# Kernel tuning notes

Measured on AMD Instinct MI355X. Metric: run time of the kernel, lower is better.

Reference implementation:

```python
import jax, jax.numpy as jnp
import numpy as np

NINP = 1024
NHID = 1024
BATCH = 16384
EPS = 1e-5


def _ln(x, g, b):
    mu = jnp.mean(x, axis=-1, keepdims=True)
    var = jnp.mean(jnp.square(x - mu), axis=-1, keepdims=True)
    return (x - mu) * jax.lax.rsqrt(var + EPS) * g + b


def setup_inputs() -> dict:
    key = jax.random.key(0)
    ks = jax.random.split(key, 12)
    s_i = 1.0 / np.sqrt(NINP)
    s_h = 1.0 / np.sqrt(NHID)
    return {
        "inp": jax.random.normal(ks[0], (BATCH, NINP), jnp.float32),
        "hidden": jax.random.normal(ks[1], (BATCH, NHID), jnp.float32),
        "W_i2gate": jax.random.uniform(ks[2], (3 * NHID, NINP), jnp.float32, -s_i, s_i),
        "b_i2gate": jnp.zeros((3 * NHID,), jnp.float32),
        "W_h2gate": jax.random.uniform(ks[3], (3 * NHID, NHID), jnp.float32, -s_h, s_h),
        "b_h2gate": jnp.zeros((3 * NHID,), jnp.float32),
        "W_i2i": jax.random.uniform(ks[4], (NHID, NINP), jnp.float32, -s_i, s_i),
        "b_i2i": jnp.zeros((NHID,), jnp.float32),
        "W_i2h": jax.random.uniform(ks[5], (NHID, NINP), jnp.float32, -s_i, s_i),
        "b_i2h": jnp.zeros((NHID,), jnp.float32),
        "W_h2h": jax.random.uniform(ks[6], (NHID, NHID), jnp.float32, -s_h, s_h),
        "b_h2h": jnp.zeros((NHID,), jnp.float32),
        "g_ig": jnp.ones((3 * NHID,), jnp.float32),
        "be_ig": jnp.zeros((3 * NHID,), jnp.float32),
        "g_hg": jnp.ones((3 * NHID,), jnp.float32),
        "be_hg": jnp.zeros((3 * NHID,), jnp.float32),
        "g_ii": jnp.ones((NHID,), jnp.float32),
        "be_ii": jnp.zeros((NHID,), jnp.float32),
        "g_ih": jnp.ones((NHID,), jnp.float32),
        "be_ih": jnp.zeros((NHID,), jnp.float32),
        "g_hh": jnp.ones((NHID,), jnp.float32),
        "be_hh": jnp.zeros((NHID,), jnp.float32),
    }


def reference(inp, hidden, W_i2gate, b_i2gate, W_h2gate, b_h2gate,
              W_i2i, b_i2i, W_i2h, b_i2h, W_h2h, b_h2h,
              g_ig, be_ig, g_hg, be_hg, g_ii, be_ii,
              g_ih, be_ih, g_hh, be_hh):
    gate = jax.nn.sigmoid(
        _ln(inp @ W_i2gate.T + b_i2gate, g_ig, be_ig)
        + _ln(hidden @ W_h2gate.T + b_h2gate, g_hg, be_hg))
    r, z, g = jnp.split(gate, 3, axis=-1)
    Hx = _ln(inp @ W_i2i.T + b_i2i, g_ii, be_ii)
    xh = _ln(inp @ W_i2h.T + b_i2h, g_ih, be_ih)
    hh = _ln(hidden @ W_h2h.T + b_h2h, g_hh, be_hh)
    hidden_m = jnp.tanh((1.0 - r) * xh + r * hh)
    return ((1.0 - z) * hidden + z * hidden_m) * (1.0 - g) + g * Hx
```

## Files before the change

kernel.cpp:

```cpp
#include <hip/hip_runtime.h>

typedef __bf16 bf16_t;
typedef bf16_t bf16x8 __attribute__((ext_vector_type(8)));
typedef bf16_t bf16x4 __attribute__((ext_vector_type(4)));
typedef float f32x4 __attribute__((ext_vector_type(4)));

#define BATCH 16384
#define KDIM  1024
#define NCOLS 9216

#define BMg 256
#define BNg 256
#define BKg 64
#define NTg (KDIM / BKg)
#define NBN (NCOLS / BNg)

__global__ __launch_bounds__(256)
void cast_all(const float* __restrict__ Wig, const float* __restrict__ Wii,
              const float* __restrict__ Wih, const float* __restrict__ Whg,
              const float* __restrict__ Whh,
              const float* __restrict__ big, const float* __restrict__ bii,
              const float* __restrict__ bih, const float* __restrict__ bhg,
              const float* __restrict__ bhh,
              const float* __restrict__ inp, const float* __restrict__ hid,
              bf16_t* __restrict__ Wcat, float* __restrict__ bcat,
              bf16_t* __restrict__ inpb, bf16_t* __restrict__ hidb,
              int nact_units, int ntot)
{
  int u = blockIdx.x * 256 + threadIdx.x;
  if (u >= ntot) return;

  if (u < 2359296) {
    const float* src; int off;
    if      (u < 786432)  { src = Wig; off = u; }
    else if (u < 1048576) { src = Wii; off = u - 786432; }
    else if (u < 1310720) { src = Wih; off = u - 1048576; }
    else if (u < 2097152) { src = Whg; off = u - 1310720; }
    else                  { src = Whh; off = u - 2097152; }
    float4 v = reinterpret_cast<const float4*>(src)[off];
    bf16x4 o;
    o[0] = (bf16_t)v.x; o[1] = (bf16_t)v.y; o[2] = (bf16_t)v.z; o[3] = (bf16_t)v.w;
    reinterpret_cast<bf16x4*>(Wcat)[u] = o;
  } else if (u < 2361600) {
    int bu = u - 2359296;
    int i = bu * 4;
    const float* src; int off;
    if      (i < 3072) { src = big; off = i; }
    else if (i < 4096) { src = bii; off = i - 3072; }
    else if (i < 5120) { src = bih; off = i - 4096; }
    else if (i < 8192) { src = bhg; off = i - 5120; }
    else               { src = bhh; off = i - 8192; }
    reinterpret_cast<float4*>(bcat)[bu] = *reinterpret_cast<const float4*>(src + off);
  } else {
    int au = u - 2361600;
    const float* src; bf16_t* dst; int off;
    if (au < nact_units) { src = inp; dst = inpb; off = au; }
    else                 { src = hid; dst = hidb; off = au - nact_units; }
    float4 v = reinterpret_cast<const float4*>(src)[off];
    bf16x4 o;
    o[0] = (bf16_t)v.x; o[1] = (bf16_t)v.y; o[2] = (bf16_t)v.z; o[3] = (bf16_t)v.w;
    reinterpret_cast<bf16x4*>(dst)[off] = o;
  }
}

__global__ __launch_bounds__(256)
void cast_acts(const float* __restrict__ inp, const float* __restrict__ hid,
               bf16_t* __restrict__ inpb, bf16_t* __restrict__ hidb, int n4) {
  int i = blockIdx.x * 256 + threadIdx.x;
  if (i >= 2 * n4) return;
  const float* src = (i < n4) ? inp : hid;
  bf16_t* dst = (i < n4) ? inpb : hidb;
  int off = (i < n4) ? i : i - n4;
  float4 v = reinterpret_cast<const float4*>(src)[off];
  bf16x4 o;
  o[0] = (bf16_t)v.x; o[1] = (bf16_t)v.y; o[2] = (bf16_t)v.z; o[3] = (bf16_t)v.w;
  reinterpret_cast<bf16x4*>(dst)[off] = o;
}

__global__ __launch_bounds__(512, 1)
void gemm_preln(const bf16_t* __restrict__ inpb, const bf16_t* __restrict__ hidb,
                const bf16_t* __restrict__ Wcat, const float* __restrict__ bcat,
                bf16_t* __restrict__ preLN, int nbm)
{
  __shared__ alignas(16) char lds_raw[131072];

  const int tid  = threadIdx.x;
  const int wid  = tid >> 6;
  const int lane = tid & 63;
  const int fr   = lane & 15;
  const int kg   = lane >> 4;
  const int wr   = wid >> 2;
  const int wc   = wid & 3;

  const int nwg = nbm * NBN;
  int orig = blockIdx.x;
  int q_ = nwg >> 3, r_ = nwg & 7, xcd = orig & 7, idx = orig >> 3;
  int wg = (xcd < r_ ? xcd * (q_ + 1) : r_ * (q_ + 1) + (xcd - r_) * q_) + idx;
  const int bm = wg / NBN, bn = wg % NBN;
  const int row0 = bm * BMg, col0 = bn * BNg;
  const bf16_t* __restrict__ act = (col0 < 5120) ? inpb : hidb;
  const bf16_t* __restrict__ wgt = Wcat + (size_t)col0 * KDIM;

  const int r_st  = tid >> 2;
  const int k8_st = (tid & 3) ^ ((r_st >> 1) & 3);
  const bf16_t* pA = act + (size_t)(row0 + r_st) * KDIM + k8_st * 8;
  const bf16_t* pB = wgt + (size_t)r_st * KDIM + k8_st * 8;

  auto stage_half = [&](int mat, int h, int T) {
    const bf16_t* s = (mat ? pB : pA) + ((size_t)h * 128) * KDIM + T * BKg;
    char* d = lds_raw + ((T & 1) << 16) + (mat << 15) + (h << 14) + (wid << 10);
    __builtin_amdgcn_global_load_lds(
        (const __attribute__((address_space(1))) unsigned int*)s,
        (__attribute__((address_space(3))) unsigned int*)d, 16, 0, 0);
    __builtin_amdgcn_global_load_lds(
        (const __attribute__((address_space(1))) unsigned int*)(s + 32),
        (__attribute__((address_space(3))) unsigned int*)(d + 8192), 16, 0, 0);
  };

  int offA[4][2], offB[2][2];
  #pragma unroll
  for (int m = 0; m < 4; ++m)
    #pragma unroll
    for (int ks = 0; ks < 2; ++ks) {
      const int rowA = wr * 64 + m * 16 + fr;
      offA[m][ks] = ks * 8192 + rowA * 64 + ((kg ^ ((rowA >> 1) & 3)) << 4);
    }
  #pragma unroll
  for (int n = 0; n < 2; ++n)
    #pragma unroll
    for (int ks = 0; ks < 2; ++ks) {
      const int rowB = wc * 32 + n * 16 + fr;
      offB[n][ks] = ks * 8192 + rowB * 64 + ((kg ^ ((rowB >> 1) & 3)) << 4);
    }

  f32x4 acc[2][4][2][2] = {};

  stage_half(0, 0, 0); stage_half(1, 0, 0);
  stage_half(0, 1, 0); stage_half(1, 1, 0);
  stage_half(0, 0, 1); stage_half(1, 0, 1);
  asm volatile("s_waitcnt vmcnt(4)" ::: "memory");
  __builtin_amdgcn_s_barrier();

  for (int T = 0; T < NTg; ++T) {
    const int bufo = (T & 1) << 16;
    #pragma unroll
    for (int ph = 0; ph < 4; ++ph) {
      const int qm = ph >> 1, qn = ph & 1;
      bf16x8 a[4][2], b[2][2];
      #pragma unroll
      for (int m = 0; m < 4; ++m)
        #pragma unroll
        for (int ks = 0; ks < 2; ++ks)
          a[m][ks] = *(const bf16x8*)(lds_raw + bufo + qm * 16384 + offA[m][ks]);
      #pragma unroll
      for (int n = 0; n < 2; ++n)
        #pragma unroll
        for (int ks = 0; ks < 2; ++ks)
          b[n][ks] = *(const bf16x8*)(lds_raw + bufo + 32768 + qn * 16384 + offB[n][ks]);

      if      (ph == 0) { if (T + 1 < NTg) stage_half(0, 1, T + 1); }
      else if (ph == 1) { if (T + 1 < NTg) stage_half(1, 1, T + 1); }
      else if (ph == 2) { if (T + 2 < NTg) stage_half(0, 0, T + 2); }
      else              { if (T + 2 < NTg) stage_half(1, 0, T + 2); }

      __builtin_amdgcn_s_barrier();
      asm volatile("s_waitcnt lgkmcnt(0)" ::: "memory");
      __builtin_amdgcn_sched_barrier(0);

      __builtin_amdgcn_s_setprio(1);
      #pragma unroll
      for (int m = 0; m < 4; ++m)
        #pragma unroll
        for (int n = 0; n < 2; ++n)
          #pragma unroll
          for (int ks = 0; ks < 2; ++ks)
            acc[qm][m][qn][n] = __builtin_amdgcn_mfma_f32_16x16x32_bf16(
                a[m][ks], b[n][ks], acc[qm][m][qn][n], 0, 0, 0);
      __builtin_amdgcn_s_setprio(0);

      if (ph < 3) __builtin_amdgcn_s_barrier();
    }
    if (T < NTg - 2) {
      asm volatile("s_waitcnt vmcnt(4)" ::: "memory");
      __builtin_amdgcn_s_barrier();
    } else if (T == NTg - 2) {
      asm volatile("s_waitcnt vmcnt(0)" ::: "memory");
      __builtin_amdgcn_s_barrier();
    }
  }

  #pragma unroll
  for (int qn_ = 0; qn_ < 2; ++qn_)
    #pragma unroll
    for (int n = 0; n < 2; ++n) {
      const int col = col0 + qn_ * 128 + wc * 32 + n * 16 + fr;
      const float bias = bcat[col];
      #pragma unroll
      for (int qm_ = 0; qm_ < 2; ++qm_)
        #pragma unroll
        for (int m = 0; m < 4; ++m) {
          const int rbase = row0 + qm_ * 128 + wr * 64 + m * 16 + kg * 4;
          #pragma unroll
          for (int j = 0; j < 4; ++j)
            preLN[(size_t)(rbase + j) * NCOLS + col] = (bf16_t)(acc[qm_][m][qn_][n][j] + bias);
        }
    }
}

__global__ __launch_bounds__(256)
void ln_combine(const bf16_t* __restrict__ preLN, const float* __restrict__ hidden,
                const float* __restrict__ g_ig, const float* __restrict__ be_ig,
                const float* __restrict__ g_hg, const float* __restrict__ be_hg,
                const float* __restrict__ g_ii, const float* __restrict__ be_ii,
                const float* __restrict__ g_ih, const float* __restrict__ be_ih,
                const float* __restrict__ g_hh, const float* __restrict__ be_hh,
                float* __restrict__ out)
{
  __shared__ alignas(16) bf16_t rowbuf[NCOLS];
  __shared__ float wsum[4][10];
  __shared__ float stats[10];
  const int tid = threadIdx.x;
  const int wv  = tid >> 6;
  const int ln  = tid & 63;
  const size_t row = blockIdx.x;
  const bf16_t* __restrict__ src = preLN + row * NCOLS;

  float s1[5] = {0.f, 0.f, 0.f, 0.f, 0.f};
  float s2[5] = {0.f, 0.f, 0.f, 0.f, 0.f};
  #pragma unroll
  for (int j = 0; j < 9; ++j) {
    const int idx = j * 1024 + tid * 4;
    bf16x4 v = *(const bf16x4*)&src[idx];
    *(bf16x4*)&rowbuf[idx] = v;
    const int sg = (j < 3) ? 0 : (j == 3) ? 1 : (j == 4) ? 2 : (j < 8) ? 3 : 4;
    const float f0 = (float)v[0], f1 = (float)v[1], f2 = (float)v[2], f3 = (float)v[3];
    s1[sg] += f0 + f1 + f2 + f3;
    s2[sg] += f0 * f0 + f1 * f1 + f2 * f2 + f3 * f3;
  }
  #pragma unroll
  for (int s = 0; s < 5; ++s)
    #pragma unroll
    for (int off = 32; off; off >>= 1) {
      s1[s] += __shfl_xor(s1[s], off);
      s2[s] += __shfl_xor(s2[s], off);
    }
  if (ln == 0) {
    #pragma unroll
    for (int s = 0; s < 5; ++s) { wsum[wv][s] = s1[s]; wsum[wv][5 + s] = s2[s]; }
  }
  __syncthreads();
  if (tid < 5) {
    const float n = (tid == 0 || tid == 3) ? 3072.f : 1024.f;
    float t1 = wsum[0][tid] + wsum[1][tid] + wsum[2][tid] + wsum[3][tid];
    float t2 = wsum[0][5 + tid] + wsum[1][5 + tid] + wsum[2][5 + tid] + wsum[3][5 + tid];
    float mu = t1 / n;
    float var = t2 / n - mu * mu;
    stats[tid] = mu;
    stats[5 + tid] = rsqrtf(var + 1e-5f);
  }
  __syncthreads();

  const float mu0 = stats[0], r0 = stats[5];
  const float mu1 = stats[1], r1 = stats[6];
  const float mu2 = stats[2], r2 = stats[7];
  const float mu3 = stats[3], r3 = stats[8];
  const float mu4 = stats[4], r4 = stats[9];
  const float* __restrict__ hrow = hidden + row * 1024;

  #pragma unroll
  for (int k = 0; k < 4; ++k) {
    const int c = tid + k * 256;
    float x_igr = (float)rowbuf[c];
    float x_igz = (float)rowbuf[c + 1024];
    float x_igg = (float)rowbuf[c + 2048];
    float x_ii  = (float)rowbuf[3072 + c];
    float x_ih  = (float)rowbuf[4096 + c];
    float x_hgr = (float)rowbuf[5120 + c];
    float x_hgz = (float)rowbuf[6144 + c];
    float x_hgg = (float)rowbuf[7168 + c];
    float x_hh  = (float)rowbuf[8192 + c];

    float pr = (x_igr - mu0) * r0 * g_ig[c]        + be_ig[c]
             + (x_hgr - mu3) * r3 * g_hg[c]        + be_hg[c];
    float pz = (x_igz - mu0) * r0 * g_ig[c + 1024] + be_ig[c + 1024]
             + (x_hgz - mu3) * r3 * g_hg[c + 1024] + be_hg[c + 1024];
    float pg = (x_igg - mu0) * r0 * g_ig[c + 2048] + be_ig[c + 2048]
             + (x_hgg - mu3) * r3 * g_hg[c + 2048] + be_hg[c + 2048];

    float rr = 1.f / (1.f + __expf(-pr));
    float zz = 1.f / (1.f + __expf(-pz));
    float gg = 1.f / (1.f + __expf(-pg));

    float Hx = (x_ii - mu1) * r1 * g_ii[c] + be_ii[c];
    float xh = (x_ih - mu2) * r2 * g_ih[c] + be_ih[c];
    float hh = (x_hh - mu4) * r4 * g_hh[c] + be_hh[c];

    float hm = tanhf((1.f - rr) * xh + rr * hh);
    float h  = hrow[c];
    out[row * 1024 + c] = ((1.f - zz) * h + zz * hm) * (1.f - gg) + gg * Hx;
  }
}

extern "C" void kernel_launch(void* const* d_in, const int* in_sizes, int n_in,
                              void* d_out, int out_size, void* d_ws, size_t ws_size,
                              hipStream_t stream) {
  const float* inp      = (const float*)d_in[0];
  const float* hidden   = (const float*)d_in[1];
  const float* W_i2gate = (const float*)d_in[2];
  const float* b_i2gate = (const float*)d_in[3];
  const float* W_h2gate = (const float*)d_in[4];
  const float* b_h2gate = (const float*)d_in[5];
  const float* W_i2i    = (const float*)d_in[6];
  const float* b_i2i    = (const float*)d_in[7];
  const float* W_i2h    = (const float*)d_in[8];
  const float* b_i2h    = (const float*)d_in[9];
  const float* W_h2h    = (const float*)d_in[10];
  const float* b_h2h    = (const float*)d_in[11];
  const float* g_ig  = (const float*)d_in[12];
  const float* be_ig = (const float*)d_in[13];
  const float* g_hg  = (const float*)d_in[14];
  const float* be_hg = (const float*)d_in[15];
  const float* g_ii  = (const float*)d_in[16];
  const float* be_ii = (const float*)d_in[17];
  const float* g_ih  = (const float*)d_in[18];
  const float* be_ih = (const float*)d_in[19];
  const float* g_hh  = (const float*)d_in[20];
  const float* be_hh = (const float*)d_in[21];
  float* out = (float*)d_out;

  const size_t WCAT_B  = (size_t)NCOLS * KDIM * 2;
  const size_t BCAT_B  = (size_t)NCOLS * 4;
  const size_t FIXED_B = WCAT_B + BCAT_B;
  const size_t PER_ROW = 2048 + 2048 + 18432;

  if (ws_size < FIXED_B + PER_ROW * 256) return;

  char* ws = (char*)d_ws;
  bf16_t* Wcat = (bf16_t*)ws;
  float*  bcat = (float*)(ws + WCAT_B);
  char*   dyn  = ws + FIXED_B;

  size_t max_rows = (ws_size - FIXED_B) / PER_ROW;
  int chunk = (int)((max_rows / 256) * 256);
  if (chunk > BATCH) chunk = BATCH;

  bf16_t* inpb  = (bf16_t*)dyn;
  bf16_t* hidb  = (bf16_t*)(dyn + (size_t)chunk * 2048);
  bf16_t* preLN = (bf16_t*)(dyn + (size_t)chunk * 4096);

  if (chunk == BATCH) {
    const int nact = BATCH * KDIM / 4;
    const int ntot = 2361600 + 2 * nact;
    cast_all<<<(ntot + 255) / 256, 256, 0, stream>>>(
        W_i2gate, W_i2i, W_i2h, W_h2gate, W_h2h,
        b_i2gate, b_i2i, b_i2h, b_h2gate, b_h2h,
        inp, hidden, Wcat, bcat, inpb, hidb, nact, ntot);

    int nbm = BATCH / BMg;
    gemm_preln<<<nbm * NBN, 512, 0, stream>>>(inpb, hidb, Wcat, bcat, preLN, nbm);

    ln_combine<<<BATCH, 256, 0, stream>>>(preLN, hidden,
                                          g_ig, be_ig, g_hg, be_hg,
                                          g_ii, be_ii, g_ih, be_ih, g_hh, be_hh,
                                          out);
  } else {
    const int ntot_w = 2361600;
    cast_all<<<(ntot_w + 255) / 256, 256, 0, stream>>>(
        W_i2gate, W_i2i, W_i2h, W_h2gate, W_h2h,
        b_i2gate, b_i2i, b_i2h, b_h2gate, b_h2h,
        nullptr, nullptr, Wcat, bcat, nullptr, nullptr, 0, ntot_w);

    for (int r0 = 0; r0 < BATCH; r0 += chunk) {
      int cr = BATCH - r0;
      if (cr > chunk) cr = chunk;
      int n4 = cr * KDIM / 4;
      cast_acts<<<(2 * n4 + 255) / 256, 256, 0, stream>>>(
          inp + (size_t)r0 * KDIM, hidden + (size_t)r0 * KDIM, inpb, hidb, n4);

      int nbm = cr / BMg;
      gemm_preln<<<nbm * NBN, 512, 0, stream>>>(inpb, hidb, Wcat, bcat, preLN, nbm);

      ln_combine<<<cr, 256, 0, stream>>>(preLN, hidden + (size_t)r0 * KDIM,
                                         g_ig, be_ig, g_hg, be_hg,
                                         g_ii, be_ii, g_ih, be_ih, g_hh, be_hh,
                                         out + (size_t)r0 * KDIM);
    }
  }
}
```

Baseline: 535.2 us.

## Reorder GEMM phases to reuse A/B fragments, raise occupancy hint, vectorize LN epilogue

The GEMM inner loop is reordered into a snake pattern (qm0qn0, qm0qn1, qm1qn1, qm1qn0), so A and B register fragments are reused across phases and fewer LDS reads are issued. The last phase also drops its lgkmcnt wait. The launch bounds are changed to request 2 waves per SIMD, which caps registers, though 128KB of LDS per block likely still limits the kernel to one block per CU. Separately, the LayerNorm/GRU epilogue is vectorized with 4-wide loads and stores, and tanhf is replaced by an exp-based formula. The register cap risks spills, and the fast tanh loses a little accuracy.

```diff
diff --git a/kernel.cpp b/kernel.cpp
--- a/kernel.cpp
+++ b/kernel.cpp
@@ -77,7 +77,7 @@
   reinterpret_cast<bf16x4*>(dst)[off] = o;
 }
 
-__global__ __launch_bounds__(512, 1)
+__global__ __launch_bounds__(512, 2)
 void gemm_preln(const bf16_t* __restrict__ inpb, const bf16_t* __restrict__ hidb,
                 const bf16_t* __restrict__ Wcat, const float* __restrict__ bcat,
                 bf16_t* __restrict__ preLN, int nbm)
@@ -143,43 +143,85 @@
 
   for (int T = 0; T < NTg; ++T) {
     const int bufo = (T & 1) << 16;
-    #pragma unroll
-    for (int ph = 0; ph < 4; ++ph) {
-      const int qm = ph >> 1, qn = ph & 1;
-      bf16x8 a[4][2], b[2][2];
-      #pragma unroll
-      for (int m = 0; m < 4; ++m)
-        #pragma unroll
-        for (int ks = 0; ks < 2; ++ks)
-          a[m][ks] = *(const bf16x8*)(lds_raw + bufo + qm * 16384 + offA[m][ks]);
+    bf16x8 a[4][2], b0[2][2], b1[2][2];
+
+    #pragma unroll
+    for (int m = 0; m < 4; ++m)
+      #pragma unroll
+      for (int ks = 0; ks < 2; ++ks)
+        a[m][ks] = *(const bf16x8*)(lds_raw + bufo + offA[m][ks]);
+    #pragma unroll
+    for (int n = 0; n < 2; ++n)
+      #pragma unroll
+      for (int ks = 0; ks < 2; ++ks)
+        b0[n][ks] = *(const bf16x8*)(lds_raw + bufo + 32768 + offB[n][ks]);
+    if (T + 1 < NTg) stage_half(0, 1, T + 1);
+    __builtin_amdgcn_s_barrier();
+    asm volatile("s_waitcnt lgkmcnt(0)" ::: "memory");
+    __builtin_amdgcn_sched_barrier(0);
+    __builtin_amdgcn_s_setprio(1);
+    #pragma unroll
+    for (int m = 0; m < 4; ++m)
       #pragma unroll
       for (int n = 0; n < 2; ++n)
         #pragma unroll
         for (int ks = 0; ks < 2; ++ks)
-          b[n][ks] = *(const bf16x8*)(lds_raw + bufo + 32768 + qn * 16384 + offB[n][ks]);
-
-      if      (ph == 0) { if (T + 1 < NTg) stage_half(0, 1, T + 1); }
-      else if (ph == 1) { if (T + 1 < NTg) stage_half(1, 1, T + 1); }
-      else if (ph == 2) { if (T + 2 < NTg) stage_half(0, 0, T + 2); }
-      else              { if (T + 2 < NTg) stage_half(1, 0, T + 2); }
-
-      __builtin_amdgcn_s_barrier();
-      asm volatile("s_waitcnt lgkmcnt(0)" ::: "memory");
-      __builtin_amdgcn_sched_barrier(0);
-
-      __builtin_amdgcn_s_setprio(1);
-      #pragma unroll
-      for (int m = 0; m < 4; ++m)
+          acc[0][m][0][n] = __builtin_amdgcn_mfma_f32_16x16x32_bf16(a[m][ks], b0[n][ks], acc[0][m][0][n], 0, 0, 0);
+    __builtin_amdgcn_s_setprio(0);
+    __builtin_amdgcn_s_barrier();
+
+    #pragma unroll
+    for (int n = 0; n < 2; ++n)
+      #pragma unroll
+      for (int ks = 0; ks < 2; ++ks)
+        b1[n][ks] = *(const bf16x8*)(lds_raw + bufo + 32768 + 16384 + offB[n][ks]);
+    if (T + 1 < NTg) stage_half(1, 1, T + 1);
+    __builtin_amdgcn_s_barrier();
+    asm volatile("s_waitcnt lgkmcnt(0)" ::: "memory");
+    __builtin_amdgcn_sched_barrier(0);
+    __builtin_amdgcn_s_setprio(1);
+    #pragma unroll
+    for (int m = 0; m < 4; ++m)
+      #pragma unroll
+      for (int n = 0; n < 2; ++n)
         #pragma unroll
-        for (int n = 0; n < 2; ++n)
-          #pragma unroll
-          for (int ks = 0; ks < 2; ++ks)
-            acc[qm][m][qn][n] = __builtin_amdgcn_mfma_f32_16x16x32_bf16(
-                a[m][ks], b[n][ks], acc[qm][m][qn][n], 0, 0, 0);
-      __builtin_amdgcn_s_setprio(0);
-
-      if (ph < 3) __builtin_amdgcn_s_barrier();
-    }
+        for (int ks = 0; ks < 2; ++ks)
+          acc[0][m][1][n] = __builtin_amdgcn_mfma_f32_16x16x32_bf16(a[m][ks], b1[n][ks], acc[0][m][1][n], 0, 0, 0);
+    __builtin_amdgcn_s_setprio(0);
+    __builtin_amdgcn_s_barrier();
+
+    #pragma unroll
+    for (int m = 0; m < 4; ++m)
+      #pragma unroll
+      for (int ks = 0; ks < 2; ++ks)
+        a[m][ks] = *(const bf16x8*)(lds_raw + bufo + 16384 + offA[m][ks]);
+    if (T + 2 < NTg) stage_half(0, 0, T + 2);
+    __builtin_amdgcn_s_barrier();
+    asm volatile("s_waitcnt lgkmcnt(0)" ::: "memory");
+    __builtin_amdgcn_sched_barrier(0);
+    __builtin_amdgcn_s_setprio(1);
+    #pragma unroll
+    for (int m = 0; m < 4; ++m)
+      #pragma unroll
+      for (int n = 0; n < 2; ++n)
+        #pragma unroll
+        for (int ks = 0; ks < 2; ++ks)
+          acc[1][m][1][n] = __builtin_amdgcn_mfma_f32_16x16x32_bf16(a[m][ks], b1[n][ks], acc[1][m][1][n], 0, 0, 0);
+    __builtin_amdgcn_s_setprio(0);
+    __builtin_amdgcn_s_barrier();
+
+    if (T + 2 < NTg) stage_half(1, 0, T + 2);
+    __builtin_amdgcn_s_barrier();
+    __builtin_amdgcn_s_setprio(1);
+    #pragma unroll
+    for (int m = 0; m < 4; ++m)
+      #pragma unroll
+      for (int n = 0; n < 2; ++n)
+        #pragma unroll
+        for (int ks = 0; ks < 2; ++ks)
+          acc[1][m][0][n] = __builtin_amdgcn_mfma_f32_16x16x32_bf16(a[m][ks], b0[n][ks], acc[1][m][0][n], 0, 0, 0);
+    __builtin_amdgcn_s_setprio(0);
+
     if (T < NTg - 2) {
       asm volatile("s_waitcnt vmcnt(4)" ::: "memory");
       __builtin_amdgcn_s_barrier();
@@ -267,38 +309,51 @@
   const float mu4 = stats[4], r4 = stats[9];
   const float* __restrict__ hrow = hidden + row * 1024;
 
-  #pragma unroll
-  for (int k = 0; k < 4; ++k) {
-    const int c = tid + k * 256;
-    float x_igr = (float)rowbuf[c];
-    float x_igz = (float)rowbuf[c + 1024];
-    float x_igg = (float)rowbuf[c + 2048];
-    float x_ii  = (float)rowbuf[3072 + c];
-    float x_ih  = (float)rowbuf[4096 + c];
-    float x_hgr = (float)rowbuf[5120 + c];
-    float x_hgz = (float)rowbuf[6144 + c];
-    float x_hgg = (float)rowbuf[7168 + c];
-    float x_hh  = (float)rowbuf[8192 + c];
-
-    float pr = (x_igr - mu0) * r0 * g_ig[c]        + be_ig[c]
-             + (x_hgr - mu3) * r3 * g_hg[c]        + be_hg[c];
-    float pz = (x_igz - mu0) * r0 * g_ig[c + 1024] + be_ig[c + 1024]
-             + (x_hgz - mu3) * r3 * g_hg[c + 1024] + be_hg[c + 1024];
-    float pg = (x_igg - mu0) * r0 * g_ig[c + 2048] + be_ig[c + 2048]
-             + (x_hgg - mu3) * r3 * g_hg[c + 2048] + be_hg[c + 2048];
+  const int c = tid * 4;
+  bf16x4 v_igr = *(const bf16x4*)&rowbuf[c];
+  bf16x4 v_igz = *(const bf16x4*)&rowbuf[c + 1024];
+  bf16x4 v_igg = *(const bf16x4*)&rowbuf[c + 2048];
+  bf16x4 v_ii  = *(const bf16x4*)&rowbuf[c + 3072];
+  bf16x4 v_ih  = *(const bf16x4*)&rowbuf[c + 4096];
+  bf16x4 v_hgr = *(const bf16x4*)&rowbuf[c + 5120];
+  bf16x4 v_hgz = *(const bf16x4*)&rowbuf[c + 6144];
+  bf16x4 v_hgg = *(const bf16x4*)&rowbuf[c + 7168];
+  bf16x4 v_hh  = *(const bf16x4*)&rowbuf[c + 8192];
+
+  f32x4 Gr  = *(const f32x4*)&g_ig[c];        f32x4 Br  = *(const f32x4*)&be_ig[c];
+  f32x4 Gz  = *(const f32x4*)&g_ig[c + 1024]; f32x4 Bz  = *(const f32x4*)&be_ig[c + 1024];
+  f32x4 Gg  = *(const f32x4*)&g_ig[c + 2048]; f32x4 Bg  = *(const f32x4*)&be_ig[c + 2048];
+  f32x4 Hr  = *(const f32x4*)&g_hg[c];        f32x4 Cr  = *(const f32x4*)&be_hg[c];
+  f32x4 Hz  = *(const f32x4*)&g_hg[c + 1024]; f32x4 Cz  = *(const f32x4*)&be_hg[c + 1024];
+  f32x4 Hg  = *(const f32x4*)&g_hg[c + 2048]; f32x4 Cg  = *(const f32x4*)&be_hg[c + 2048];
+  f32x4 Gii = *(const f32x4*)&g_ii[c];        f32x4 Bii = *(const f32x4*)&be_ii[c];
+  f32x4 Gih = *(const f32x4*)&g_ih[c];        f32x4 Bih = *(const f32x4*)&be_ih[c];
+  f32x4 Ghh = *(const f32x4*)&g_hh[c];        f32x4 Bhh = *(const f32x4*)&be_hh[c];
+  f32x4 hv  = *(const f32x4*)&hrow[c];
+
+  f32x4 o;
+  #pragma unroll
+  for (int i = 0; i < 4; ++i) {
+    float pr = ((float)v_igr[i] - mu0) * r0 * Gr[i] + Br[i]
+             + ((float)v_hgr[i] - mu3) * r3 * Hr[i] + Cr[i];
+    float pz = ((float)v_igz[i] - mu0) * r0 * Gz[i] + Bz[i]
+             + ((float)v_hgz[i] - mu3) * r3 * Hz[i] + Cz[i];
+    float pg = ((float)v_igg[i] - mu0) * r0 * Gg[i] + Bg[i]
+             + ((float)v_hgg[i] - mu3) * r3 * Hg[i] + Cg[i];
 
     float rr = 1.f / (1.f + __expf(-pr));
     float zz = 1.f / (1.f + __expf(-pz));
     float gg = 1.f / (1.f + __expf(-pg));
 
-    float Hx = (x_ii - mu1) * r1 * g_ii[c] + be_ii[c];
-    float xh = (x_ih - mu2) * r2 * g_ih[c] + be_ih[c];
-    float hh = (x_hh - mu4) * r4 * g_hh[c] + be_hh[c];
-
-    float hm = tanhf((1.f - rr) * xh + rr * hh);
-    float h  = hrow[c];
-    out[row * 1024 + c] = ((1.f - zz) * h + zz * hm) * (1.f - gg) + gg * Hx;
-  }
+    float Hx = ((float)v_ii[i] - mu1) * r1 * Gii[i] + Bii[i];
+    float xh = ((float)v_ih[i] - mu2) * r2 * Gih[i] + Bih[i];
+    float hh = ((float)v_hh[i] - mu4) * r4 * Ghh[i] + Bhh[i];
+
+    float pre = (1.f - rr) * xh + rr * hh;
+    float hm  = 1.f - 2.f / (1.f + __expf(2.f * pre));
+    o[i] = ((1.f - zz) * hv[i] + zz * hm) * (1.f - gg) + gg * Hx;
+  }
+  *(f32x4*)&out[row * 1024 + c] = o;
 }
 
 extern "C" void kernel_launch(void* const* d_in, const int* in_sizes, int n_in,
```

Result: faster. 499.7 us (-6.6%).
